# Kernel optimization log

Hardware: AMD Instinct MI355X
Metric: run time of the kernel (lower is better)

Reference implementation:

```python
import jax, jax.numpy as jnp
import numpy as np

WIN = 32  # hardcoded window size in the original module


def _find(parent, x):
    while parent[x] != x:
        parent[x] = parent[parent[x]]
        x = parent[x]
    return x


def _label_background(bg):
    # 4-connected component labeling of True pixels; False pixels get label 0
    w = bg.shape[0]
    n = w * w
    parent = np.arange(n, dtype=np.int64)
    flat = bg.ravel()
    idx = np.arange(n).reshape(w, w)
    e1 = np.concatenate([idx[:, :-1].ravel(), idx[:-1, :].ravel()])
    e2 = np.concatenate([idx[:, 1:].ravel(), idx[1:, :].ravel()])
    for a, b in zip(e1, e2):
        if flat[a] and flat[b]:
            ra, rb = _find(parent, a), _find(parent, b)
            if ra != rb:
                parent[ra] = rb
    labels = np.zeros(n, dtype=np.int64)
    root2lab = {}
    nxt = 1
    for i in range(n):
        if flat[i]:
            r = _find(parent, i)
            if r not in root2lab:
                root2lab[r] = nxt
                nxt += 1
            labels[i] = root2lab[r]
    return labels


def _malis(seg, e1, e2, costs, pos):
    # Kruskal-style maximin MALIS edge weighting (descending affinity order).
    # Pairs involving segment label 0 (foreground / non-background) are excluded.
    n = seg.shape[0]
    parent = np.arange(n, dtype=np.int64)
    cnts = [({int(seg[i]): 1} if seg[i] != 0 else {}) for i in range(n)]
    w = np.zeros(costs.shape[0], dtype=np.int64)
    order = np.argsort(-costs, kind='stable')
    for e in order:
        a, b = _find(parent, e1[e]), _find(parent, e2[e])
        if a == b:
            continue
        ca, cb = cnts[a], cnts[b]
        if len(ca) > len(cb):  # small-to-large merge
            a, b, ca, cb = b, a, cb, ca
        common = 0
        for l, c in ca.items():
            if l in cb:
                common += c * cb[l]
        if pos:
            w[e] = common
        else:
            sa = sum(ca.values())
            sb = sum(cb.values())
            w[e] = sa * sb - common
        for l, c in ca.items():
            cb[l] = cb.get(l, 0) + c
        parent[a] = b
        cnts[a] = {}
    return w


def _malis_weights_full(pred, target):
    pred = np.asarray(pred)
    target = np.asarray(target)
    B, C, H, W = pred.shape
    weights_n = np.zeros(pred.shape, dtype=np.float32)
    weights_p = np.zeros(pred.shape, dtype=np.float32)
    idx = np.arange(WIN * WIN).reshape(WIN, WIN)
    e1 = np.concatenate([idx[:, :-1].ravel(), idx[:-1, :].ravel()])
    e2 = np.concatenate([idx[:, 1:].ravel(), idx[1:, :].ravel()])
    for r in range(H // WIN):
        for c in range(W // WIN):
            p = pred[:, :, r * WIN:(r + 1) * WIN, c * WIN:(c + 1) * WIN]
            t = target[:, :, r * WIN:(r + 1) * WIN, c * WIN:(c + 1) * WIN]
            costs_h = (p[:, :, :, :-1] + p[:, :, :, 1:]).reshape(B, -1)
            costs_v = (p[:, :, :-1, :] + p[:, :, 1:, :]).reshape(B, -1)
            costs = np.concatenate([costs_h, costs_v], 1)
            gt_h = (t[:, :, :, :-1] + t[:, :, :, 1:]).reshape(B, -1)
            gt_v = (t[:, :, :-1, :] + t[:, :, 1:, :]).reshape(B, -1)
            gt = np.concatenate([gt_h, gt_v], 1)
            costs_n = costs.copy()
            costs_p = costs.copy()
            costs_n[gt > 20] = 20
            costs_p[gt < 10] = 0
            gt = np.minimum(gt, 20)
            for i in range(B):
                seg = _label_background(t[i, 0] == 0)
                wn = _malis(seg, e1, e2, costs_n[i].astype(np.float32), 0).astype(np.float64)
                wp = _malis(seg, e1, e2, costs_p[i].astype(np.float32), 1).astype(np.float64)
                if wn.sum() > 0:
                    wn = wn / wn.sum()
                if wp.sum() > 0:
                    wp = wp / wp.sum()
                wn[gt[i] >= 10] = 0
                wp[gt[i] < 20] = 0
                half = WIN * (WIN - 1)
                for wsrc, wdst in ((wn, weights_n), (wp, weights_p)):
                    wh = wsrc[:half].reshape(WIN, WIN - 1)
                    wv = wsrc[half:].reshape(WIN - 1, WIN)
                    nw = np.zeros((WIN, WIN), dtype=np.float64)
                    nw[:, :-1] += wh
                    nw[:, 1:] += wh
                    nw[:-1, :] += wv
                    nw[1:, :] += wv
                    wdst[i, 0, r * WIN:(r + 1) * WIN, c * WIN:(c + 1) * WIN] = nw
    return weights_n, weights_p


def setup_inputs() -> dict:
    key = jax.random.key(0)
    k1, k2 = jax.random.split(key)
    y_true = jax.random.randint(k1, (4, 1, 256, 256), 0, 2).astype(jnp.float32) * 20.0
    y_pred = jax.random.uniform(k2, (4, 1, 256, 256), dtype=jnp.float32) * 20.0
    return {"y_true": y_true, "y_pred": y_pred}


def reference(y_true, y_pred):
    malis_lr = 1.0
    malis_lr_pos = 1.0
    out_sd = (jax.ShapeDtypeStruct(y_pred.shape, jnp.float32),
              jax.ShapeDtypeStruct(y_pred.shape, jnp.float32))
    weights_n, weights_p = jax.pure_callback(
        _malis_weights_full, out_sd,
        jax.lax.stop_gradient(y_pred), jax.lax.stop_gradient(y_true))
    loss_n = y_pred ** 2
    loss_p = (20.0 - y_pred) ** 2
    return (malis_lr * loss_n * weights_n + malis_lr_pos * loss_p * weights_p).sum()
```

## Files before the change

### kernel.cpp

```cpp
#include <hip/hip_runtime.h>

#define NPIX   1024
#define NEH    992
#define NEDGE  1984
#define SORTN  2048
#define CHUNK  8
#define NMERGE 1023
#define NIL    0xFFFFu

#define MRG_STRIDE 20480
#define MRG_M      0
#define MRG_RA     256
#define MRG_RB     4608
#define MRG_SS     8960
#define MRG_ED     13312
#define MRG_NXT    15616

__device__ __forceinline__ void edge_ab(int e, int& a, int& b) {
    if (e < NEH) { int y = e / 31; int x = e - y * 31; a = y * 32 + x; b = a + 1; }
    else         { int ev = e - NEH; a = ev; b = ev + 32; }
}

__device__ __forceinline__ uint4 add4(uint4 x, uint4 y) {
    return make_uint4(x.x + y.x, x.y + y.y, x.z + y.z, x.w + y.w);
}
__device__ __forceinline__ uint4 sub4(uint4 x, uint4 y) {
    return make_uint4(x.x - y.x, x.y - y.y, x.z - y.z, x.w - y.w);
}

__device__ __forceinline__ unsigned rdl32(unsigned v, int lane) {
    return (unsigned)__builtin_amdgcn_readlane((int)v, lane);
}
__device__ __forceinline__ unsigned long long rdl64(unsigned long long v, int lane) {
    unsigned lo = (unsigned)__builtin_amdgcn_readlane((int)(unsigned)v, lane);
    unsigned hi = (unsigned)__builtin_amdgcn_readlane((int)(unsigned)(v >> 32), lane);
    return ((unsigned long long)hi << 32) | lo;
}

__device__ void ccl_body(char* smem, int* kprimeSh,
                         const float* __restrict__ t_glob,
                         unsigned short* __restrict__ pixLab_g,
                         int* __restrict__ Kg, int tileId) {
    const int tid = threadIdx.x;
    const int bat = tileId >> 6;
    const int tile = tileId & 63;
    const int tr = tile >> 3, tc = tile & 7;

    unsigned short* labS = (unsigned short*)smem;
    unsigned int*   cntS = (unsigned int*)(smem + 2048);
    unsigned char*  bgS  = (unsigned char*)(smem + 20480);

    for (int i = tid; i < NPIX; i += 256) {
        int y = i >> 5, x = i & 31;
        int gidx = bat * 65536 + (tr * 32 + y) * 256 + (tc * 32 + x);
        bgS[i] = (t_glob[gidx] == 0.0f) ? 1 : 0;
    }
    __syncthreads();

    if (tid < 64) {
        const int lane = tid;
        if (lane < 32) {
            #pragma unroll
            for (int x = 0; x < 32; x++) {
                int i = lane * 32 + x;
                labS[i] = bgS[i] ? (unsigned short)i : (unsigned short)NIL;
            }
        }
        while (true) {
            bool changed = false;
            if (lane < 32) {
                const int base = lane * 32;
                unsigned short v[32];
                #pragma unroll
                for (int x = 0; x < 32; x++) v[x] = labS[base + x];
                unsigned run = NIL;
                #pragma unroll
                for (int x = 0; x < 32; x++) {
                    unsigned val = v[x];
                    if (val == NIL) { run = NIL; }
                    else { unsigned nv = min(run, val); changed |= (nv != val); v[x] = (unsigned short)nv; run = nv; }
                }
                run = NIL;
                #pragma unroll
                for (int x = 31; x >= 0; x--) {
                    unsigned val = v[x];
                    if (val == NIL) { run = NIL; }
                    else { unsigned nv = min(run, val); changed |= (nv != val); v[x] = (unsigned short)nv; run = nv; }
                }
                #pragma unroll
                for (int x = 0; x < 32; x++) labS[base + x] = v[x];
            }
            if (lane < 32) {
                unsigned short c[32];
                #pragma unroll
                for (int k = 0; k < 32; k++) c[k] = labS[k * 32 + lane];
                unsigned run = NIL;
                #pragma unroll
                for (int k = 0; k < 32; k++) {
                    unsigned val = c[k];
                    if (val == NIL) { run = NIL; }
                    else { unsigned nv = min(run, val); changed |= (nv != val); c[k] = (unsigned short)nv; run = nv; }
                }
                run = NIL;
                #pragma unroll
                for (int k = 31; k >= 0; k--) {
                    unsigned val = c[k];
                    if (val == NIL) { run = NIL; }
                    else { unsigned nv = min(run, val); changed |= (nv != val); c[k] = (unsigned short)nv; run = nv; }
                }
                #pragma unroll
                for (int k = 0; k < 32; k++) labS[k * 32 + lane] = c[k];
            }
            if (!__any(changed)) break;
        }
    }
    __syncthreads();

    for (int i = tid; i < NPIX; i += 256) cntS[i] = 0;
    if (tid == 0) *kprimeSh = 0;
    __syncthreads();
    for (int i = tid; i < NPIX; i += 256)
        if (bgS[i]) atomicAdd(&cntS[labS[i]], 1u);
    __syncthreads();
    for (int i = tid; i < NPIX; i += 256) {
        if (bgS[i] && (int)labS[i] == i) {
            unsigned id = (cntS[i] >= 2) ? (unsigned)atomicAdd(kprimeSh, 1) : NIL;
            cntS[i] = id;
        }
    }
    __syncthreads();
    for (int i = tid; i < NPIX; i += 256)
        pixLab_g[tileId * NPIX + i] = bgS[i] ? (unsigned short)cntS[labS[i]] : (unsigned short)NIL;
    if (tid == 0) Kg[tileId] = *kprimeSh;
}

__device__ void sort_body(char* smem,
                          const float* __restrict__ t_glob,
                          const float* __restrict__ p_glob,
                          unsigned short* __restrict__ ord_g, int wg) {
    const int tid = threadIdx.x;
    const int sgn = wg & 1;
    const int tileId = wg >> 1;
    const int bat = tileId >> 6;
    const int tile = tileId & 63;
    const int tr = tile >> 3, tc = tile & 7;

    float*              pT   = (float*)smem;
    unsigned long long* keys = (unsigned long long*)(smem + 4096);
    unsigned char*      bgS  = (unsigned char*)(smem + 20480);

    for (int i = tid; i < NPIX; i += 256) {
        int y = i >> 5, x = i & 31;
        int gidx = bat * 65536 + (tr * 32 + y) * 256 + (tc * 32 + x);
        pT[i] = p_glob[gidx];
        bgS[i] = (t_glob[gidx] == 0.0f) ? 1 : 0;
    }
    __syncthreads();

    for (int k = tid; k < SORTN; k += 256) {
        unsigned long long key = 0ULL;
        if (k < NEDGE) {
            int a, b; edge_ab(k, a, b);
            float cost = pT[a] + pT[b];
            int nfg = (int)(!bgS[a]) + (int)(!bgS[b]);
            if (sgn == 0) { if (nfg == 2) cost = 20.0f; }
            else          { if (nfg == 0) cost = 0.0f;  }
            key = ((unsigned long long)__float_as_uint(cost) << 16)
                | (unsigned long long)(0xFFFFu - (unsigned)k);
        }
        keys[k] = key;
    }
    __syncthreads();
    for (int kk = 2; kk <= SORTN; kk <<= 1) {
        for (int jj = kk >> 1; jj > 0; jj >>= 1) {
            for (int i = tid; i < SORTN; i += 256) {
                int ixj = i ^ jj;
                if (ixj > i) {
                    unsigned long long A = keys[i], Bv = keys[ixj];
                    bool descBlk = ((i & kk) == 0);
                    if ((A < Bv) == descBlk) { keys[i] = Bv; keys[ixj] = A; }
                }
            }
            __syncthreads();
        }
    }
    for (int k = tid; k < NEDGE; k += 256)
        ord_g[(size_t)wg * SORTN + k] = (unsigned short)(0xFFFFu - (unsigned)(keys[k] & 0xFFFFULL));
}

__global__ __launch_bounds__(256, 2)
void k12_ccl_sort(const float* __restrict__ t_glob,
                  const float* __restrict__ p_glob,
                  unsigned short* __restrict__ pixLab_g,
                  int* __restrict__ Kg,
                  unsigned short* __restrict__ ord_g,
                  int nT) {
    __shared__ __align__(16) char smem[21504];
    __shared__ int kprimeSh;
    if ((int)blockIdx.x < nT)
        ccl_body(smem, &kprimeSh, t_glob, pixLab_g, Kg, blockIdx.x);
    else
        sort_body(smem, t_glob, p_glob, ord_g, blockIdx.x - nT);
}

__global__ __launch_bounds__(64)
void k3_kruskal(const float* __restrict__ t_glob,
                const unsigned short* __restrict__ ord_g,
                char* __restrict__ mrg_base) {
    const int lane = threadIdx.x;
    const int wg  = blockIdx.x;
    const int tileId = wg >> 1;
    const int bat = tileId >> 6;
    const int tile = tileId & 63;
    const int tr = tile >> 3, tc = tile & 7;

    __shared__ unsigned short parentS[NPIX];
    __shared__ unsigned long long nodeS[NPIX];
    __shared__ unsigned short nextS[NPIX];
    __shared__ unsigned int   claimS[NPIX];

    char* mg = mrg_base + (size_t)wg * MRG_STRIDE;
    unsigned int*   mrA = (unsigned int*)(mg + MRG_RA);
    unsigned int*   mrB = (unsigned int*)(mg + MRG_RB);
    unsigned int*   mSS = (unsigned int*)(mg + MRG_SS);
    unsigned short* mED = (unsigned short*)(mg + MRG_ED);
    unsigned short* mNX = (unsigned short*)(mg + MRG_NXT);
    const unsigned short* ord = ord_g + (size_t)wg * SORTN;

    for (int i = lane; i < NPIX; i += 64) {
        int y = i >> 5, x = i & 31;
        int gidx = bat * 65536 + (tr * 32 + y) * 256 + (tc * 32 + x);
        unsigned bg = (t_glob[gidx] == 0.0f) ? 1u : 0u;
        parentS[i] = (unsigned short)i;
        nodeS[i] = ((unsigned long long)i << 48) | ((unsigned long long)i << 32)
                 | (1ULL << 16) | (unsigned long long)bg;
        nextS[i] = (unsigned short)NIL;
    }
    __syncthreads();

    int m = 0;
    for (int kb = 0; kb < NEDGE; kb += 64) {
        int e = ord[kb + lane];
        int a, b; edge_ab(e, a, b);
        unsigned ra = (unsigned)a, rb = (unsigned)b;
        while (true) {
            unsigned pa = parentS[ra];
            unsigned pb = parentS[rb];
            if (pa == ra && pb == rb) break;
            if (pa != ra) { unsigned ga = parentS[pa]; parentS[ra] = (unsigned short)ga; ra = ga; }
            if (pb != rb) { unsigned gb = parentS[pb]; parentS[rb] = (unsigned short)gb; rb = gb; }
        }
        bool pending = (ra != rb);
        bool committed = false;
        unsigned recA = 0, recB = 0, recSS = 0;

        int winners = 64;
        while (__any(pending) && winners >= 6) {
            if (pending) {
                claimS[ra] = 0xFFFFFFFFu;
                claimS[rb] = 0xFFFFFFFFu;
            }
            if (pending) {
                atomicMin(&claimS[ra], (unsigned)lane);
                atomicMin(&claimS[rb], (unsigned)lane);
            }
            bool win = pending && (claimS[ra] == (unsigned)lane) && (claimS[rb] == (unsigned)lane);
            if (win) {
                unsigned long long nA = nodeS[ra], nB = nodeS[rb];
                unsigned cons = ra, surv = rb;
                unsigned szAu = (unsigned)(nA >> 16) & 0xFFFFu;
                unsigned szBu = (unsigned)(nB >> 16) & 0xFFFFu;
                if (szAu > szBu) {
                    unsigned t = cons; cons = surv; surv = t;
                    unsigned long long tn = nA; nA = nB; nB = tn;
                }
                unsigned headA = (unsigned)(nA >> 48);
                unsigned tailA = (unsigned)(nA >> 32) & 0xFFFFu;
                unsigned szA   = (unsigned)(nA >> 16) & 0xFFFFu;
                unsigned slA   = (unsigned)nA & 0xFFFFu;
                unsigned headB = (unsigned)(nB >> 48);
                unsigned tailB = (unsigned)(nB >> 32) & 0xFFFFu;
                unsigned szB   = (unsigned)(nB >> 16) & 0xFFFFu;
                unsigned slB   = (unsigned)nB & 0xFFFFu;
                unsigned long long merged =
                      ((unsigned long long)headA << 48)
                    | ((unsigned long long)tailB << 32)
                    | ((unsigned long long)(szA + szB) << 16)
                    | (unsigned long long)(slA + slB);
                parentS[cons] = (unsigned short)surv;
                nodeS[surv]   = merged;
                nextS[tailA]  = (unsigned short)headB;
                recA = (headA << 16) | headB;
                recB = (szA << 16) | szB;
                recSS = slA * slB;
                committed = true;
                pending = false;
            }
            winners = (int)__popcll(__ballot(win));
            if (pending) {
                while (true) {
                    unsigned pa = parentS[ra];
                    unsigned pb = parentS[rb];
                    if (pa == ra && pb == rb) break;
                    if (pa != ra) { unsigned ga = parentS[pa]; parentS[ra] = (unsigned short)ga; ra = ga; }
                    if (pb != rb) { unsigned gb = parentS[pb]; parentS[rb] = (unsigned short)gb; rb = gb; }
                }
                if (ra == rb) pending = false;
            }
        }

        unsigned long long cmB = __ballot(committed);
        if (committed) {
            int idx = m + (int)__popcll(cmB & ((1ULL << lane) - 1ULL));
            mrA[idx] = recA;
            mrB[idx] = recB;
            mSS[idx] = recSS;
            mED[idx] = (unsigned short)e;
        }
        int bulkCount = (int)__popcll(cmB);

        int logCount = 0;
        if (__any(pending)) {
            unsigned long long na = 0, nb = 0;
            if (pending) { na = nodeS[ra]; nb = nodeS[rb]; }
            unsigned specAB = (ra << 16) | rb;
            unsigned long long candm = __ballot(pending);
            unsigned logRa  = 0xFFFFFFFFu;
            unsigned logRbO = 0xFFFFFFFFu;
            unsigned curRoot = 0xFFFFFFFFu;
            unsigned long long logNode = 0;
            while (candm != 0ULL) {
                int j = __ffsll((long long)candm) - 1;
                candm &= candm - 1ULL;
                unsigned sAB = rdl32(specAB, j);
                unsigned cra = sAB >> 16;
                unsigned crb = sAB & 0xFFFFu;
                unsigned long long hitA = __ballot(logRa == cra);
                unsigned long long hitB = __ballot(logRa == crb);
                if (hitA) cra = rdl32(curRoot, __ffsll((long long)hitA) - 1);
                if (hitB) crb = rdl32(curRoot, __ffsll((long long)hitB) - 1);
                if (cra == crb) continue;
                unsigned ce = rdl32((unsigned)e, j);
                unsigned long long hbA = __ballot(logRbO == cra);
                unsigned long long hbB = __ballot(logRbO == crb);
                unsigned long long cna = hbA ? rdl64(logNode, 63 - __clzll((long long)hbA)) : rdl64(na, j);
                unsigned long long cnb = hbB ? rdl64(logNode, 63 - __clzll((long long)hbB)) : rdl64(nb, j);
                unsigned cons = cra, surv = crb;
                unsigned szAq = (unsigned)(cna >> 16) & 0xFFFFu;
                unsigned szBq = (unsigned)(cnb >> 16) & 0xFFFFu;
                if (szAq > szBq) {
                    unsigned t = cons; cons = surv; surv = t;
                    unsigned long long tn = cna; cna = cnb; cnb = tn;
                }
                unsigned headA = (unsigned)(cna >> 48);
                unsigned tailA = (unsigned)(cna >> 32) & 0xFFFFu;
                unsigned szA   = (unsigned)(cna >> 16) & 0xFFFFu;
                unsigned slA   = (unsigned)cna & 0xFFFFu;
                unsigned headB = (unsigned)(cnb >> 48);
                unsigned tailB = (unsigned)(cnb >> 32) & 0xFFFFu;
                unsigned szB   = (unsigned)(cnb >> 16) & 0xFFFFu;
                unsigned slB   = (unsigned)cnb & 0xFFFFu;
                unsigned long long merged =
                      ((unsigned long long)headA << 48)
                    | ((unsigned long long)tailB << 32)
                    | ((unsigned long long)(szA + szB) << 16)
                    | (unsigned long long)(slA + slB);
                if (curRoot == cons) curRoot = surv;
                if (lane == logCount) {
                    logRa = cons; logRbO = surv; curRoot = surv; logNode = merged;
                    parentS[cons] = (unsigned short)surv;
                    nodeS[surv]   = merged;
                    nextS[tailA]  = (unsigned short)headB;
                    int idx = m + bulkCount + logCount;
                    mrA[idx] = (headA << 16) | headB;
                    mrB[idx] = (szA << 16) | szB;
                    mSS[idx] = slA * slB;
                    mED[idx] = (unsigned short)ce;
                }
                logCount++;
            }
        }
        m += bulkCount + logCount;
    }
    if (lane == 0) *(int*)(mg + MRG_M) = m;
    for (int i = lane; i < NPIX; i += 64) mNX[i] = nextS[i];
}

__global__ __launch_bounds__(256, 2)
void k4_weights(const float* __restrict__ t_glob,
                const float* __restrict__ p_glob,
                const unsigned short* __restrict__ pixLab_g,
                const int* __restrict__ Kg,
                const char* __restrict__ mrg_base,
                float* __restrict__ out) {
    const int tid = threadIdx.x;
    const int wg  = blockIdx.x;
    const int sgn = wg & 1;
    const int tileId = wg >> 1;
    const int bat = tileId >> 6;
    const int tile = tileId & 63;
    const int tr = tile >> 3, tc = tile & 7;

    __shared__ float          pT[NPIX];
    __shared__ unsigned char  bgS[NPIX];
    __shared__ unsigned short pixLab[NPIX];
    __shared__ unsigned short posS[NPIX];
    __shared__ unsigned int   mRecA[NMERGE];
    __shared__ unsigned int   mRecB[NMERGE];
    __shared__ unsigned int   mSaSb[NMERGE];
    __shared__ unsigned int   commonW[NMERGE];
    __shared__ unsigned short mEd[NMERGE];
    __shared__ __align__(16) unsigned long long big[2564];
    __shared__ unsigned wsumSh;
    __shared__ float lossSh;

    const char* mg = mrg_base + (size_t)wg * MRG_STRIDE;
    const int M = *(const int*)(mg + MRG_M);
    const int K = Kg[tileId];
    const unsigned int*   mrA = (const unsigned int*)(mg + MRG_RA);
    const unsigned int*   mrB = (const unsigned int*)(mg + MRG_RB);
    const unsigned int*   mSS = (const unsigned int*)(mg + MRG_SS);
    const unsigned short* mED = (const unsigned short*)(mg + MRG_ED);
    const unsigned short* mNX = (const unsigned short*)(mg + MRG_NXT);

    for (int i = tid; i < NPIX; i += 256) {
        int y = i >> 5, x = i & 31;
        int gidx = bat * 65536 + (tr * 32 + y) * 256 + (tc * 32 + x);
        pT[i] = p_glob[gidx];
        bgS[i] = (t_glob[gidx] == 0.0f) ? 1 : 0;
        pixLab[i] = pixLab_g[tileId * NPIX + i];
    }
    for (int j = tid; j < M; j += 256) {
        mRecA[j] = mrA[j];
        mRecB[j] = mrB[j];
        mSaSb[j] = mSS[j];
        mEd[j]   = mED[j];
        commonW[j] = 0;
    }

    unsigned short* n0 = (unsigned short*)big;
    unsigned short* n1 = n0 + 1024;
    unsigned short* d0 = n0 + 2048;
    unsigned short* d1 = n0 + 3072;
    for (int i = tid; i < NPIX; i += 256) { n0[i] = mNX[i]; d0[i] = 1; }
    __syncthreads();
    for (int s = 0; s < 10; s++) {
        unsigned short* sn = (s & 1) ? n1 : n0;
        unsigned short* sd = (s & 1) ? d1 : d0;
        unsigned short* dn = (s & 1) ? n0 : n1;
        unsigned short* dd = (s & 1) ? d0 : d1;
        for (int i = tid; i < NPIX; i += 256) {
            unsigned nx = sn[i];
            unsigned dv = sd[i];
            if (nx != NIL) { dv += sd[nx]; nx = sn[nx]; }
            dn[i] = (unsigned short)nx;
            dd[i] = (unsigned short)dv;
        }
        __syncthreads();
    }
    for (int i = tid; i < NPIX; i += 256)
        posS[i] = (unsigned short)(NPIX - (int)d0[i]);
    __syncthreads();

    unsigned*       P32 = (unsigned*)big;
    uint4*          P4  = (uint4*)big;
    unsigned*       scr = P32 + 4100;
    uint4*          S4  = (uint4*)scr;
    unsigned short* P16 = (unsigned short*)big;
    for (int base = 0; base < K; base += CHUNK) {
        for (int idx = tid; idx < 4100; idx += 256) P32[idx] = 0;
        __syncthreads();
        for (int i = tid; i < NPIX; i += 256) {
            unsigned l = pixLab[i];
            if (l != NIL && l >= (unsigned)base && l < (unsigned)(base + CHUNK))
                P16[(posS[i] + 1) * 8 + (l - base)] = 1;
        }
        __syncthreads();
        {
            int r0 = tid * 4 + 1;
            uint4 acc = P4[r0];
            for (int rr = r0 + 1; rr <= r0 + 3; rr++) { acc = add4(acc, P4[rr]); P4[rr] = acc; }
            S4[tid] = acc;
            __syncthreads();
            if (tid < 64) {
                uint4 s0 = S4[tid * 4], s1 = S4[tid * 4 + 1], s2 = S4[tid * 4 + 2], s3 = S4[tid * 4 + 3];
                uint4 t1 = add4(s0, s1), t2 = add4(t1, s2), t3 = add4(t2, s3);
                uint4 run = t3;
                #pragma unroll
                for (int d = 1; d < 64; d <<= 1) {
                    uint4 o;
                    o.x = __shfl_up(run.x, d, 64);
                    o.y = __shfl_up(run.y, d, 64);
                    o.z = __shfl_up(run.z, d, 64);
                    o.w = __shfl_up(run.w, d, 64);
                    if (tid >= d) run = add4(run, o);
                }
                uint4 off = sub4(run, t3);
                S4[tid * 4]     = add4(s0, off);
                S4[tid * 4 + 1] = add4(t1, off);
                S4[tid * 4 + 2] = add4(t2, off);
                S4[tid * 4 + 3] = add4(t3, off);
            }
            __syncthreads();
            if (tid > 0) {
                uint4 off = S4[tid - 1];
                for (int rr = r0; rr <= r0 + 3; rr++) P4[rr] = add4(P4[rr], off);
            }
        }
        __syncthreads();
        for (int j = tid; j < M; j += 256) {
            unsigned recA = mRecA[j], recB = mRecB[j];
            unsigned aS = posS[recA >> 16];
            unsigned bS = posS[recA & 0xFFFFu];
            uint4 da = sub4(P4[aS + (recB >> 16)], P4[aS]);
            uint4 db = sub4(P4[bS + (recB & 0xFFFFu)], P4[bS]);
            unsigned acc;
            acc  = (da.x & 0xFFFFu) * (db.x & 0xFFFFu) + (da.x >> 16) * (db.x >> 16);
            acc += (da.y & 0xFFFFu) * (db.y & 0xFFFFu) + (da.y >> 16) * (db.y >> 16);
            acc += (da.z & 0xFFFFu) * (db.z & 0xFFFFu) + (da.z >> 16) * (db.z >> 16);
            acc += (da.w & 0xFFFFu) * (db.w & 0xFFFFu) + (da.w >> 16) * (db.w >> 16);
            commonW[j] += acc;
        }
        __syncthreads();
    }

    if (tid == 0) { wsumSh = 0; lossSh = 0.0f; }
    __syncthreads();
    unsigned wloc = 0;
    for (int j = tid; j < M; j += 256)
        wloc += (sgn == 0) ? (mSaSb[j] - commonW[j]) : commonW[j];
    if (wloc) atomicAdd(&wsumSh, wloc);
    __syncthreads();
    const unsigned wsum = wsumSh;
    if (wsum > 0) {
        const double inv = 1.0 / (double)wsum;
        float lloc = 0.0f;
        for (int j = tid; j < M; j += 256) {
            unsigned w = (sgn == 0) ? (mSaSb[j] - commonW[j]) : commonW[j];
            if (!w) continue;
            int e = mEd[j];
            int a, b; edge_ab(e, a, b);
            int nfg = (int)(!bgS[a]) + (int)(!bgS[b]);
            bool keep = (sgn == 0) ? (nfg == 0) : (nfg >= 1);
            if (!keep) continue;
            float wn = (float)((double)w * inv);
            float fa, fb;
            if (sgn == 0) { fa = pT[a] * pT[a];            fb = pT[b] * pT[b]; }
            else { float da = 20.0f - pT[a], db = 20.0f - pT[b]; fa = da * da; fb = db * db; }
            lloc += wn * (fa + fb);
        }
        if (lloc != 0.0f) atomicAdd(&lossSh, lloc);
        __syncthreads();
        if (tid == 0 && lossSh != 0.0f) atomicAdd(out, lossSh);
    }
}

__global__ __launch_bounds__(256, 2)
void malis_mono(const float* __restrict__ t_glob,
                const float* __restrict__ p_glob,
                float* __restrict__ out) {
    const int tid  = threadIdx.x;
    const int wg   = blockIdx.x;
    const int sgn  = wg & 1;
    const int tileId = wg >> 1;
    const int bat  = tileId >> 6;
    const int tile = tileId & 63;
    const int tr = tile >> 3, tc = tile & 7;

    __shared__ float          pT[NPIX];
    __shared__ unsigned char  bgS[NPIX];
    __shared__ unsigned short pixLab[NPIX];
    __shared__ unsigned short parentS[NPIX];
    __shared__ unsigned short nextS[NPIX];
    __shared__ unsigned long long nodeS[NPIX];
    __shared__ unsigned int   claimS[NPIX];
    __shared__ unsigned short posS[NPIX];
    __shared__ unsigned short orderS[NEDGE];
    __shared__ unsigned int   mRecA[NMERGE];
    __shared__ unsigned int   mRecB[NMERGE];
    __shared__ unsigned short mEd[NMERGE];
    __shared__ unsigned int   mSaSb[NMERGE];
    __shared__ unsigned int   commonW[NMERGE];
    __shared__ __align__(16) unsigned long long big[2564];
    __shared__ int   kprimeSh, mCountSh;
    __shared__ unsigned wsumSh;
    __shared__ float lossSh;

    for (int i = tid; i < NPIX; i += 256) {
        int y = i >> 5, x = i & 31;
        int gidx = bat * 65536 + (tr * 32 + y) * 256 + (tc * 32 + x);
        pT[i] = p_glob[gidx];
        bgS[i] = (t_glob[gidx] == 0.0f) ? 1 : 0;
    }
    __syncthreads();

    unsigned short* labS = (unsigned short*)big;
    unsigned int*   cntS = (unsigned int*)(((char*)big) + 2048);
    if (tid < 64) {
        const int lane = tid;
        if (lane < 32) {
            #pragma unroll
            for (int x = 0; x < 32; x++) {
                int i = lane * 32 + x;
                labS[i] = bgS[i] ? (unsigned short)i : (unsigned short)NIL;
            }
        }
        while (true) {
            bool changed = false;
            if (lane < 32) {
                const int base = lane * 32;
                unsigned short v[32];
                #pragma unroll
                for (int x = 0; x < 32; x++) v[x] = labS[base + x];
                unsigned run = NIL;
                #pragma unroll
                for (int x = 0; x < 32; x++) {
                    unsigned val = v[x];
                    if (val == NIL) { run = NIL; }
                    else { unsigned nv = min(run, val); changed |= (nv != val); v[x] = (unsigned short)nv; run = nv; }
                }
                run = NIL;
                #pragma unroll
                for (int x = 31; x >= 0; x--) {
                    unsigned val = v[x];
                    if (val == NIL) { run = NIL; }
                    else { unsigned nv = min(run, val); changed |= (nv != val); v[x] = (unsigned short)nv; run = nv; }
                }
                #pragma unroll
                for (int x = 0; x < 32; x++) labS[base + x] = v[x];
            }
            if (lane < 32) {
                unsigned short c[32];
                #pragma unroll
                for (int k = 0; k < 32; k++) c[k] = labS[k * 32 + lane];
                unsigned run = NIL;
                #pragma unroll
                for (int k = 0; k < 32; k++) {
                    unsigned val = c[k];
                    if (val == NIL) { run = NIL; }
                    else { unsigned nv = min(run, val); changed |= (nv != val); c[k] = (unsigned short)nv; run = nv; }
                }
                run = NIL;
                #pragma unroll
                for (int k = 31; k >= 0; k--) {
                    unsigned val = c[k];
                    if (val == NIL) { run = NIL; }
                    else { unsigned nv = min(run, val); changed |= (nv != val); c[k] = (unsigned short)nv; run = nv; }
                }
                #pragma unroll
                for (int k = 0; k < 32; k++) labS[k * 32 + lane] = c[k];
            }
            if (!__any(changed)) break;
        }
    }
    __syncthreads();

    for (int i = tid; i < NPIX; i += 256) cntS[i] = 0;
    if (tid == 0) kprimeSh = 0;
    __syncthreads();
    for (int i = tid; i < NPIX; i += 256)
        if (bgS[i]) atomicAdd(&cntS[labS[i]], 1u);
    __syncthreads();
    for (int i = tid; i < NPIX; i += 256) {
        if (bgS[i] && (int)labS[i] == i) {
            unsigned id = (cntS[i] >= 2) ? (unsigned)atomicAdd(&kprimeSh, 1) : NIL;
            cntS[i] = id;
        }
    }
    __syncthreads();
    for (int i = tid; i < NPIX; i += 256)
        pixLab[i] = bgS[i] ? (unsigned short)cntS[labS[i]] : (unsigned short)NIL;
    __syncthreads();
    const int K = kprimeSh;

    unsigned long long* keys = big;
    for (int k = tid; k < SORTN; k += 256) {
        unsigned long long key = 0ULL;
        if (k < NEDGE) {
            int a, b; edge_ab(k, a, b);
            float cost = pT[a] + pT[b];
            int nfg = (int)(!bgS[a]) + (int)(!bgS[b]);
            if (sgn == 0) { if (nfg == 2) cost = 20.0f; }
            else          { if (nfg == 0) cost = 0.0f;  }
            key = ((unsigned long long)__float_as_uint(cost) << 16)
                | (unsigned long long)(0xFFFFu - (unsigned)k);
        }
        keys[k] = key;
    }
    __syncthreads();
    for (int kk = 2; kk <= SORTN; kk <<= 1) {
        for (int jj = kk >> 1; jj > 0; jj >>= 1) {
            for (int i = tid; i < SORTN; i += 256) {
                int ixj = i ^ jj;
                if (ixj > i) {
                    unsigned long long A = keys[i], Bv = keys[ixj];
                    bool descBlk = ((i & kk) == 0);
                    if ((A < Bv) == descBlk) { keys[i] = Bv; keys[ixj] = A; }
                }
            }
            __syncthreads();
        }
    }
    for (int k = tid; k < NEDGE; k += 256)
        orderS[k] = (unsigned short)(0xFFFFu - (unsigned)(keys[k] & 0xFFFFULL));
    for (int i = tid; i < NPIX; i += 256) {
        parentS[i] = (unsigned short)i;
        nodeS[i] = ((unsigned long long)i << 48) | ((unsigned long long)i << 32)
                 | (1ULL << 16) | (unsigned long long)bgS[i];
        nextS[i] = (unsigned short)NIL;
    }
    __syncthreads();

    if (tid < 64) {
        const int lane = tid;
        int m = 0;
        for (int kb = 0; kb < NEDGE; kb += 64) {
            int e = orderS[kb + lane];
            int a, b; edge_ab(e, a, b);
            unsigned ra = (unsigned)a, rb = (unsigned)b;
            bool pending = true;
            bool committed = false;
            unsigned recA = 0, recB = 0, recSS = 0;
            while (__any(pending)) {
                if (pending) {
                    while (true) {
                        unsigned pa = parentS[ra];
                        unsigned pb = parentS[rb];
                        if (pa == ra && pb == rb) break;
                        if (pa != ra) { unsigned ga = parentS[pa]; parentS[ra] = (unsigned short)ga; ra = ga; }
                        if (pb != rb) { unsigned gb = parentS[pb]; parentS[rb] = (unsigned short)gb; rb = gb; }
                    }
                    if (ra == rb) pending = false;
                }
                if (pending) {
                    claimS[ra] = 0xFFFFFFFFu;
                    claimS[rb] = 0xFFFFFFFFu;
                }
                if (pending) {
                    atomicMin(&claimS[ra], (unsigned)lane);
                    atomicMin(&claimS[rb], (unsigned)lane);
                }
                bool win = pending && (claimS[ra] == (unsigned)lane) && (claimS[rb] == (unsigned)lane);
                if (win) {
                    unsigned long long nA = nodeS[ra], nB = nodeS[rb];
                    unsigned cons = ra, surv = rb;
                    unsigned szAu = (unsigned)(nA >> 16) & 0xFFFFu;
                    unsigned szBu = (unsigned)(nB >> 16) & 0xFFFFu;
                    if (szAu > szBu) {
                        unsigned t = cons; cons = surv; surv = t;
                        unsigned long long tn = nA; nA = nB; nB = tn;
                    }
                    unsigned headA = (unsigned)(nA >> 48);
                    unsigned tailA = (unsigned)(nA >> 32) & 0xFFFFu;
                    unsigned szA   = (unsigned)(nA >> 16) & 0xFFFFu;
                    unsigned slA   = (unsigned)nA & 0xFFFFu;
                    unsigned headB = (unsigned)(nB >> 48);
                    unsigned tailB = (unsigned)(nB >> 32) & 0xFFFFu;
                    unsigned szB   = (unsigned)(nB >> 16) & 0xFFFFu;
                    unsigned slB   = (unsigned)nB & 0xFFFFu;
                    unsigned long long merged =
                          ((unsigned long long)headA << 48)
                        | ((unsigned long long)tailB << 32)
                        | ((unsigned long long)(szA + szB) << 16)
                        | (unsigned long long)(slA + slB);
                    parentS[cons] = (unsigned short)surv;
                    nodeS[surv]   = merged;
                    nextS[tailA]  = (unsigned short)headB;
                    recA = (headA << 16) | headB;
                    recB = (szA << 16) | szB;
                    recSS = slA * slB;
                    committed = true;
                    pending = false;
                }
            }
            unsigned long long cm = __ballot(committed);
            if (committed) {
                int idx = m + (int)__popcll(cm & ((1ULL << lane) - 1ULL));
                mRecA[idx] = recA;
                mRecB[idx] = recB;
                mSaSb[idx] = recSS;
                mEd[idx]   = (unsigned short)e;
            }
            m += (int)__popcll(cm);
        }
        if (lane == 0) mCountSh = m;
    }
    __syncthreads();
    const int M = mCountSh;
    for (int j = tid; j < M; j += 256) commonW[j] = 0;

    unsigned short* n0 = (unsigned short*)big;
    unsigned short* n1 = n0 + 1024;
    unsigned short* d0 = n0 + 2048;
    unsigned short* d1 = n0 + 3072;
    for (int i = tid; i < NPIX; i += 256) { n0[i] = nextS[i]; d0[i] = 1; }
    __syncthreads();
    for (int s = 0; s < 10; s++) {
        unsigned short* sn = (s & 1) ? n1 : n0;
        unsigned short* sd = (s & 1) ? d1 : d0;
        unsigned short* dn = (s & 1) ? n0 : n1;
        unsigned short* dd = (s & 1) ? d0 : d1;
        for (int i = tid; i < NPIX; i += 256) {
            unsigned nx = sn[i];
            unsigned dv = sd[i];
            if (nx != NIL) { dv += sd[nx]; nx = sn[nx]; }
            dn[i] = (unsigned short)nx;
            dd[i] = (unsigned short)dv;
        }
        __syncthreads();
    }
    for (int i = tid; i < NPIX; i += 256)
        posS[i] = (unsigned short)(NPIX - (int)d0[i]);
    __syncthreads();

    unsigned*       P32 = (unsigned*)big;
    uint4*          P4  = (uint4*)big;
    unsigned*       scr = P32 + 4100;
    uint4*          S4  = (uint4*)scr;
    unsigned short* P16 = (unsigned short*)big;
    for (int base = 0; base < K; base += CHUNK) {
        for (int idx = tid; idx < 4100; idx += 256) P32[idx] = 0;
        __syncthreads();
        for (int i = tid; i < NPIX; i += 256) {
            unsigned l = pixLab[i];
            if (l != NIL && l >= (unsigned)base && l < (unsigned)(base + CHUNK))
                P16[(posS[i] + 1) * 8 + (l - base)] = 1;
        }
        __syncthreads();
        {
            int r0 = tid * 4 + 1;
            uint4 acc = P4[r0];
            for (int rr = r0 + 1; rr <= r0 + 3; rr++) { acc = add4(acc, P4[rr]); P4[rr] = acc; }
            S4[tid] = acc;
            __syncthreads();
            if (tid < 64) {
                uint4 s0 = S4[tid * 4], s1 = S4[tid * 4 + 1], s2 = S4[tid * 4 + 2], s3 = S4[tid * 4 + 3];
                uint4 t1 = add4(s0, s1), t2 = add4(t1, s2), t3 = add4(t2, s3);
                uint4 run = t3;
                #pragma unroll
                for (int d = 1; d < 64; d <<= 1) {
                    uint4 o;
                    o.x = __shfl_up(run.x, d, 64);
                    o.y = __shfl_up(run.y, d, 64);
                    o.z = __shfl_up(run.z, d, 64);
                    o.w = __shfl_up(run.w, d, 64);
                    if (tid >= d) run = add4(run, o);
                }
                uint4 off = sub4(run, t3);
                S4[tid * 4]     = add4(s0, off);
                S4[tid * 4 + 1] = add4(t1, off);
                S4[tid * 4 + 2] = add4(t2, off);
                S4[tid * 4 + 3] = add4(t3, off);
            }
            __syncthreads();
            if (tid > 0) {
                uint4 off = S4[tid - 1];
                for (int rr = r0; rr <= r0 + 3; rr++) P4[rr] = add4(P4[rr], off);
            }
        }
        __syncthreads();
        for (int j = tid; j < M; j += 256) {
            unsigned recA = mRecA[j], recB = mRecB[j];
            unsigned aS = posS[recA >> 16];
            unsigned bS = posS[recA & 0xFFFFu];
            uint4 da = sub4(P4[aS + (recB >> 16)], P4[aS]);
            uint4 db = sub4(P4[bS + (recB & 0xFFFFu)], P4[bS]);
            unsigned acc;
            acc  = (da.x & 0xFFFFu) * (db.x & 0xFFFFu) + (da.x >> 16) * (db.x >> 16);
            acc += (da.y & 0xFFFFu) * (db.y & 0xFFFFu) + (da.y >> 16) * (db.y >> 16);
            acc += (da.z & 0xFFFFu) * (db.z & 0xFFFFu) + (da.z >> 16) * (db.z >> 16);
            acc += (da.w & 0xFFFFu) * (db.w & 0xFFFFu) + (da.w >> 16) * (db.w >> 16);
            commonW[j] += acc;
        }
        __syncthreads();
    }

    if (tid == 0) { wsumSh = 0; lossSh = 0.0f; }
    __syncthreads();
    unsigned wloc = 0;
    for (int j = tid; j < M; j += 256)
        wloc += (sgn == 0) ? (mSaSb[j] - commonW[j]) : commonW[j];
    if (wloc) atomicAdd(&wsumSh, wloc);
    __syncthreads();
    const unsigned wsum = wsumSh;
    if (wsum > 0) {
        const double inv = 1.0 / (double)wsum;
        float lloc = 0.0f;
        for (int j = tid; j < M; j += 256) {
            unsigned w = (sgn == 0) ? (mSaSb[j] - commonW[j]) : commonW[j];
            if (!w) continue;
            int e = mEd[j];
            int a, b; edge_ab(e, a, b);
            int nfg = (int)(!bgS[a]) + (int)(!bgS[b]);
            bool keep = (sgn == 0) ? (nfg == 0) : (nfg >= 1);
            if (!keep) continue;
            float wn = (float)((double)w * inv);
            float fa, fb;
            if (sgn == 0) { fa = pT[a] * pT[a];            fb = pT[b] * pT[b]; }
            else { float da = 20.0f - pT[a], db = 20.0f - pT[b]; fa = da * da; fb = db * db; }
            lloc += wn * (fa + fb);
        }
        if (lloc != 0.0f) atomicAdd(&lossSh, lloc);
        __syncthreads();
        if (tid == 0 && lossSh != 0.0f) atomicAdd(out, lossSh);
    }
}

extern "C" void kernel_launch(void* const* d_in, const int* in_sizes, int n_in,
                              void* d_out, int out_size, void* d_ws, size_t ws_size,
                              hipStream_t stream) {
    const float* y_true = (const float*)d_in[0];
    const float* y_pred = (const float*)d_in[1];
    float* out = (float*)d_out;
    const int B  = in_sizes[0] / (256 * 256);
    const int nT = B * 64;
    const int nW = nT * 2;

    const size_t offK   = (size_t)nT * 2048;
    const size_t offOrd = offK + (((size_t)nT * 4 + 255) & ~(size_t)255);
    const size_t offMrg = offOrd + (size_t)nW * 4096;
    const size_t need   = offMrg + (size_t)nW * MRG_STRIDE;

    hipMemsetAsync(d_out, 0, (size_t)out_size * sizeof(float), stream);

    if (ws_size >= need) {
        char* ws = (char*)d_ws;
        unsigned short* pixLab_g = (unsigned short*)ws;
        int*            Kg       = (int*)(ws + offK);
        unsigned short* ord_g    = (unsigned short*)(ws + offOrd);
        char*           mrg      = ws + offMrg;
        hipLaunchKernelGGL(k12_ccl_sort, dim3(nT + nW), dim3(256), 0, stream,
                           y_true, y_pred, pixLab_g, Kg, ord_g, nT);
        hipLaunchKernelGGL(k3_kruskal,   dim3(nW), dim3(64),  0, stream, y_true, ord_g, mrg);
        hipLaunchKernelGGL(k4_weights,   dim3(nW), dim3(256), 0, stream, y_true, y_pred,
                           pixLab_g, Kg, mrg, out);
    } else {
        hipLaunchKernelGGL(malis_mono, dim3(nW), dim3(256), 0, stream, y_true, y_pred, out);
    }
}
```

Baseline: 297.6 us.

## Fuse Kruskal pass into weights kernel and add star-merge fast path

Merges the single-wave Kruskal kernel into the weights kernel, so the merge records and next-list stay in shared memory instead of being written to and re-read from a global workspace, and one kernel launch goes away. Claim slots now carry a generation counter, so they are no longer reset each round. A new fast path handles the case where every leftover pending edge touches one common root: it merges them all in one step using prefix sums instead of a serial lane-by-lane loop. Costs: the fused kernel uses more shared memory, which can lower occupancy, and 192 of the 256 threads sit idle during the serial Kruskal phase.

After: 270.8 us. 1.1x faster.

```diff
diff --git a/kernel.cpp b/kernel.cpp
--- a/kernel.cpp
+++ b/kernel.cpp
@@ -7,14 +7,6 @@
 #define CHUNK  8
 #define NMERGE 1023
 #define NIL    0xFFFFu
-
-#define MRG_STRIDE 20480
-#define MRG_M      0
-#define MRG_RA     256
-#define MRG_RB     4608
-#define MRG_SS     8960
-#define MRG_ED     13312
-#define MRG_NXT    15616
 
 __device__ __forceinline__ void edge_ab(int e, int& a, int& b) {
     if (e < NEH) { int y = e / 31; int x = e - y * 31; a = y * 32 + x; b = a + 1; }
@@ -203,196 +195,13 @@
         sort_body(smem, t_glob, p_glob, ord_g, blockIdx.x - nT);
 }
 
-__global__ __launch_bounds__(64)
-void k3_kruskal(const float* __restrict__ t_glob,
-                const unsigned short* __restrict__ ord_g,
-                char* __restrict__ mrg_base) {
-    const int lane = threadIdx.x;
-    const int wg  = blockIdx.x;
-    const int tileId = wg >> 1;
-    const int bat = tileId >> 6;
-    const int tile = tileId & 63;
-    const int tr = tile >> 3, tc = tile & 7;
-
-    __shared__ unsigned short parentS[NPIX];
-    __shared__ unsigned long long nodeS[NPIX];
-    __shared__ unsigned short nextS[NPIX];
-    __shared__ unsigned int   claimS[NPIX];
-
-    char* mg = mrg_base + (size_t)wg * MRG_STRIDE;
-    unsigned int*   mrA = (unsigned int*)(mg + MRG_RA);
-    unsigned int*   mrB = (unsigned int*)(mg + MRG_RB);
-    unsigned int*   mSS = (unsigned int*)(mg + MRG_SS);
-    unsigned short* mED = (unsigned short*)(mg + MRG_ED);
-    unsigned short* mNX = (unsigned short*)(mg + MRG_NXT);
-    const unsigned short* ord = ord_g + (size_t)wg * SORTN;
-
-    for (int i = lane; i < NPIX; i += 64) {
-        int y = i >> 5, x = i & 31;
-        int gidx = bat * 65536 + (tr * 32 + y) * 256 + (tc * 32 + x);
-        unsigned bg = (t_glob[gidx] == 0.0f) ? 1u : 0u;
-        parentS[i] = (unsigned short)i;
-        nodeS[i] = ((unsigned long long)i << 48) | ((unsigned long long)i << 32)
-                 | (1ULL << 16) | (unsigned long long)bg;
-        nextS[i] = (unsigned short)NIL;
-    }
-    __syncthreads();
-
-    int m = 0;
-    for (int kb = 0; kb < NEDGE; kb += 64) {
-        int e = ord[kb + lane];
-        int a, b; edge_ab(e, a, b);
-        unsigned ra = (unsigned)a, rb = (unsigned)b;
-        while (true) {
-            unsigned pa = parentS[ra];
-            unsigned pb = parentS[rb];
-            if (pa == ra && pb == rb) break;
-            if (pa != ra) { unsigned ga = parentS[pa]; parentS[ra] = (unsigned short)ga; ra = ga; }
-            if (pb != rb) { unsigned gb = parentS[pb]; parentS[rb] = (unsigned short)gb; rb = gb; }
-        }
-        bool pending = (ra != rb);
-        bool committed = false;
-        unsigned recA = 0, recB = 0, recSS = 0;
-
-        int winners = 64;
-        while (__any(pending) && winners >= 6) {
-            if (pending) {
-                claimS[ra] = 0xFFFFFFFFu;
-                claimS[rb] = 0xFFFFFFFFu;
-            }
-            if (pending) {
-                atomicMin(&claimS[ra], (unsigned)lane);
-                atomicMin(&claimS[rb], (unsigned)lane);
-            }
-            bool win = pending && (claimS[ra] == (unsigned)lane) && (claimS[rb] == (unsigned)lane);
-            if (win) {
-                unsigned long long nA = nodeS[ra], nB = nodeS[rb];
-                unsigned cons = ra, surv = rb;
-                unsigned szAu = (unsigned)(nA >> 16) & 0xFFFFu;
-                unsigned szBu = (unsigned)(nB >> 16) & 0xFFFFu;
-                if (szAu > szBu) {
-                    unsigned t = cons; cons = surv; surv = t;
-                    unsigned long long tn = nA; nA = nB; nB = tn;
-                }
-                unsigned headA = (unsigned)(nA >> 48);
-                unsigned tailA = (unsigned)(nA >> 32) & 0xFFFFu;
-                unsigned szA   = (unsigned)(nA >> 16) & 0xFFFFu;
-                unsigned slA   = (unsigned)nA & 0xFFFFu;
-                unsigned headB = (unsigned)(nB >> 48);
-                unsigned tailB = (unsigned)(nB >> 32) & 0xFFFFu;
-                unsigned szB   = (unsigned)(nB >> 16) & 0xFFFFu;
-                unsigned slB   = (unsigned)nB & 0xFFFFu;
-                unsigned long long merged =
-                      ((unsigned long long)headA << 48)
-                    | ((unsigned long long)tailB << 32)
-                    | ((unsigned long long)(szA + szB) << 16)
-                    | (unsigned long long)(slA + slB);
-                parentS[cons] = (unsigned short)surv;
-                nodeS[surv]   = merged;
-                nextS[tailA]  = (unsigned short)headB;
-                recA = (headA << 16) | headB;
-                recB = (szA << 16) | szB;
-                recSS = slA * slB;
-                committed = true;
-                pending = false;
-            }
-            winners = (int)__popcll(__ballot(win));
-            if (pending) {
-                while (true) {
-                    unsigned pa = parentS[ra];
-                    unsigned pb = parentS[rb];
-                    if (pa == ra && pb == rb) break;
-                    if (pa != ra) { unsigned ga = parentS[pa]; parentS[ra] = (unsigned short)ga; ra = ga; }
-                    if (pb != rb) { unsigned gb = parentS[pb]; parentS[rb] = (unsigned short)gb; rb = gb; }
-                }
-                if (ra == rb) pending = false;
-            }
-        }
-
-        unsigned long long cmB = __ballot(committed);
-        if (committed) {
-            int idx = m + (int)__popcll(cmB & ((1ULL << lane) - 1ULL));
-            mrA[idx] = recA;
-            mrB[idx] = recB;
-            mSS[idx] = recSS;
-            mED[idx] = (unsigned short)e;
-        }
-        int bulkCount = (int)__popcll(cmB);
-
-        int logCount = 0;
-        if (__any(pending)) {
-            unsigned long long na = 0, nb = 0;
-            if (pending) { na = nodeS[ra]; nb = nodeS[rb]; }
-            unsigned specAB = (ra << 16) | rb;
-            unsigned long long candm = __ballot(pending);
-            unsigned logRa  = 0xFFFFFFFFu;
-            unsigned logRbO = 0xFFFFFFFFu;
-            unsigned curRoot = 0xFFFFFFFFu;
-            unsigned long long logNode = 0;
-            while (candm != 0ULL) {
-                int j = __ffsll((long long)candm) - 1;
-                candm &= candm - 1ULL;
-                unsigned sAB = rdl32(specAB, j);
-                unsigned cra = sAB >> 16;
-                unsigned crb = sAB & 0xFFFFu;
-                unsigned long long hitA = __ballot(logRa == cra);
-                unsigned long long hitB = __ballot(logRa == crb);
-                if (hitA) cra = rdl32(curRoot, __ffsll((long long)hitA) - 1);
-                if (hitB) crb = rdl32(curRoot, __ffsll((long long)hitB) - 1);
-                if (cra == crb) continue;
-                unsigned ce = rdl32((unsigned)e, j);
-                unsigned long long hbA = __ballot(logRbO == cra);
-                unsigned long long hbB = __ballot(logRbO == crb);
-                unsigned long long cna = hbA ? rdl64(logNode, 63 - __clzll((long long)hbA)) : rdl64(na, j);
-                unsigned long long cnb = hbB ? rdl64(logNode, 63 - __clzll((long long)hbB)) : rdl64(nb, j);
-                unsigned cons = cra, surv = crb;
-                unsigned szAq = (unsigned)(cna >> 16) & 0xFFFFu;
-                unsigned szBq = (unsigned)(cnb >> 16) & 0xFFFFu;
-                if (szAq > szBq) {
-                    unsigned t = cons; cons = surv; surv = t;
-                    unsigned long long tn = cna; cna = cnb; cnb = tn;
-                }
-                unsigned headA = (unsigned)(cna >> 48);
-                unsigned tailA = (unsigned)(cna >> 32) & 0xFFFFu;
-                unsigned szA   = (unsigned)(cna >> 16) & 0xFFFFu;
-                unsigned slA   = (unsigned)cna & 0xFFFFu;
-                unsigned headB = (unsigned)(cnb >> 48);
-                unsigned tailB = (unsigned)(cnb >> 32) & 0xFFFFu;
-                unsigned szB   = (unsigned)(cnb >> 16) & 0xFFFFu;
-                unsigned slB   = (unsigned)cnb & 0xFFFFu;
-                unsigned long long merged =
-                      ((unsigned long long)headA << 48)
-                    | ((unsigned long long)tailB << 32)
-                    | ((unsigned long long)(szA + szB) << 16)
-                    | (unsigned long long)(slA + slB);
-                if (curRoot == cons) curRoot = surv;
-                if (lane == logCount) {
-                    logRa = cons; logRbO = surv; curRoot = surv; logNode = merged;
-                    parentS[cons] = (unsigned short)surv;
-                    nodeS[surv]   = merged;
-                    nextS[tailA]  = (unsigned short)headB;
-                    int idx = m + bulkCount + logCount;
-                    mrA[idx] = (headA << 16) | headB;
-                    mrB[idx] = (szA << 16) | szB;
-                    mSS[idx] = slA * slB;
-                    mED[idx] = (unsigned short)ce;
-                }
-                logCount++;
-            }
-        }
-        m += bulkCount + logCount;
-    }
-    if (lane == 0) *(int*)(mg + MRG_M) = m;
-    for (int i = lane; i < NPIX; i += 64) mNX[i] = nextS[i];
-}
-
 __global__ __launch_bounds__(256, 2)
-void k4_weights(const float* __restrict__ t_glob,
-                const float* __restrict__ p_glob,
-                const unsigned short* __restrict__ pixLab_g,
-                const int* __restrict__ Kg,
-                const char* __restrict__ mrg_base,
-                float* __restrict__ out) {
+void k34_fused(const float* __restrict__ t_glob,
+               const float* __restrict__ p_glob,
+               const unsigned short* __restrict__ pixLab_g,
+               const int* __restrict__ Kg,
+               const unsigned short* __restrict__ ord_g,
+               float* __restrict__ out) {
     const int tid = threadIdx.x;
     const int wg  = blockIdx.x;
     const int sgn = wg & 1;
@@ -401,48 +210,261 @@
     const int tile = tileId & 63;
     const int tr = tile >> 3, tc = tile & 7;
 
-    __shared__ float          pT[NPIX];
-    __shared__ unsigned char  bgS[NPIX];
-    __shared__ unsigned short pixLab[NPIX];
-    __shared__ unsigned short posS[NPIX];
+    __shared__ unsigned short parentS[NPIX];
+    __shared__ unsigned long long nodeS[NPIX];
+    __shared__ unsigned short nextS[NPIX];
     __shared__ unsigned int   mRecA[NMERGE];
     __shared__ unsigned int   mRecB[NMERGE];
     __shared__ unsigned int   mSaSb[NMERGE];
     __shared__ unsigned int   commonW[NMERGE];
     __shared__ unsigned short mEd[NMERGE];
+    __shared__ float          pT[NPIX];
+    __shared__ unsigned char  bgS[NPIX];
+    __shared__ unsigned short pixLab[NPIX];
+    __shared__ unsigned short posS[NPIX];
+    __shared__ unsigned int   claimS[NPIX];
     __shared__ __align__(16) unsigned long long big[2564];
+    __shared__ int   mCountSh;
     __shared__ unsigned wsumSh;
     __shared__ float lossSh;
 
-    const char* mg = mrg_base + (size_t)wg * MRG_STRIDE;
-    const int M = *(const int*)(mg + MRG_M);
-    const int K = Kg[tileId];
-    const unsigned int*   mrA = (const unsigned int*)(mg + MRG_RA);
-    const unsigned int*   mrB = (const unsigned int*)(mg + MRG_RB);
-    const unsigned int*   mSS = (const unsigned int*)(mg + MRG_SS);
-    const unsigned short* mED = (const unsigned short*)(mg + MRG_ED);
-    const unsigned short* mNX = (const unsigned short*)(mg + MRG_NXT);
+    const unsigned short* ord = ord_g + (size_t)wg * SORTN;
 
     for (int i = tid; i < NPIX; i += 256) {
         int y = i >> 5, x = i & 31;
         int gidx = bat * 65536 + (tr * 32 + y) * 256 + (tc * 32 + x);
+        float tv = t_glob[gidx];
+        unsigned bg = (tv == 0.0f) ? 1u : 0u;
         pT[i] = p_glob[gidx];
-        bgS[i] = (t_glob[gidx] == 0.0f) ? 1 : 0;
+        bgS[i] = (unsigned char)bg;
         pixLab[i] = pixLab_g[tileId * NPIX + i];
-    }
-    for (int j = tid; j < M; j += 256) {
-        mRecA[j] = mrA[j];
-        mRecB[j] = mrB[j];
-        mSaSb[j] = mSS[j];
-        mEd[j]   = mED[j];
-        commonW[j] = 0;
-    }
+        parentS[i] = (unsigned short)i;
+        nodeS[i] = ((unsigned long long)i << 48) | ((unsigned long long)i << 32)
+                 | (1ULL << 16) | (unsigned long long)bg;
+        nextS[i] = (unsigned short)NIL;
+        claimS[i] = 0xFFFFFFFFu;
+    }
+    __syncthreads();
+
+    if (tid < 64) {
+        const int lane = tid;
+        int m = 0;
+        unsigned gen = 1u << 24;
+        for (int kb = 0; kb < NEDGE; kb += 64) {
+            int e = ord[kb + lane];
+            int a, b; edge_ab(e, a, b);
+            unsigned ra = (unsigned)a, rb = (unsigned)b;
+            while (true) {
+                unsigned pa = parentS[ra];
+                unsigned pb = parentS[rb];
+                if (pa == ra && pb == rb) break;
+                if (pa != ra) { unsigned ga = parentS[pa]; parentS[ra] = (unsigned short)ga; ra = ga; }
+                if (pb != rb) { unsigned gb = parentS[pb]; parentS[rb] = (unsigned short)gb; rb = gb; }
+            }
+            bool pending = (ra != rb);
+            bool committed = false;
+            unsigned recA = 0, recB = 0, recSS = 0;
+
+            int winners = 64;
+            while (__any(pending) && winners >= 6) {
+                gen--;
+                unsigned myval = (gen << 6) | (unsigned)lane;
+                if (pending) {
+                    atomicMin(&claimS[ra], myval);
+                    atomicMin(&claimS[rb], myval);
+                }
+                bool win = pending && (claimS[ra] == myval) && (claimS[rb] == myval);
+                if (win) {
+                    unsigned long long nA = nodeS[ra], nB = nodeS[rb];
+                    unsigned cons = ra, surv = rb;
+                    unsigned szAu = (unsigned)(nA >> 16) & 0xFFFFu;
+                    unsigned szBu = (unsigned)(nB >> 16) & 0xFFFFu;
+                    if (szAu > szBu) {
+                        unsigned t = cons; cons = surv; surv = t;
+                        unsigned long long tn = nA; nA = nB; nB = tn;
+                    }
+                    unsigned headA = (unsigned)(nA >> 48);
+                    unsigned tailA = (unsigned)(nA >> 32) & 0xFFFFu;
+                    unsigned szA   = (unsigned)(nA >> 16) & 0xFFFFu;
+                    unsigned slA   = (unsigned)nA & 0xFFFFu;
+                    unsigned headB = (unsigned)(nB >> 48);
+                    unsigned tailB = (unsigned)(nB >> 32) & 0xFFFFu;
+                    unsigned szB   = (unsigned)(nB >> 16) & 0xFFFFu;
+                    unsigned slB   = (unsigned)nB & 0xFFFFu;
+                    unsigned long long merged =
+                          ((unsigned long long)headA << 48)
+                        | ((unsigned long long)tailB << 32)
+                        | ((unsigned long long)(szA + szB) << 16)
+                        | (unsigned long long)(slA + slB);
+                    parentS[cons] = (unsigned short)surv;
+                    nodeS[surv]   = merged;
+                    nextS[tailA]  = (unsigned short)headB;
+                    recA = (headA << 16) | headB;
+                    recB = (szA << 16) | szB;
+                    recSS = slA * slB;
+                    committed = true;
+                    pending = false;
+                }
+                winners = (int)__popcll(__ballot(win));
+                if (pending) {
+                    while (true) {
+                        unsigned pa = parentS[ra];
+                        unsigned pb = parentS[rb];
+                        if (pa == ra && pb == rb) break;
+                        if (pa != ra) { unsigned ga = parentS[pa]; parentS[ra] = (unsigned short)ga; ra = ga; }
+                        if (pb != rb) { unsigned gb = parentS[pb]; parentS[rb] = (unsigned short)gb; rb = gb; }
+                    }
+                    if (ra == rb) pending = false;
+                }
+            }
+
+            unsigned long long cmB = __ballot(committed);
+            if (committed) {
+                int idx = m + (int)__popcll(cmB & ((1ULL << lane) - 1ULL));
+                mRecA[idx] = recA;
+                mRecB[idx] = recB;
+                mSaSb[idx] = recSS;
+                mEd[idx]   = (unsigned short)e;
+            }
+            m += (int)__popcll(cmB);
+
+            int logCount = 0;
+            unsigned long long candm0 = __ballot(pending);
+            if (candm0 != 0ULL) {
+                unsigned long long na = 0, nb = 0;
+                if (pending) { na = nodeS[ra]; nb = nodeS[rb]; }
+                int j0 = __ffsll((long long)candm0) - 1;
+                unsigned Ra = rdl32(ra, j0), Rb = rdl32(rb, j0);
+                unsigned long long mAc = __ballot(pending && (ra == Ra || rb == Ra));
+                unsigned long long mBc = __ballot(pending && (ra == Rb || rb == Rb));
+                unsigned R = (__popcll(mAc) >= __popcll(mBc)) ? Ra : Rb;
+                bool onR  = pending && ((ra == R) != (rb == R));
+                bool offR = pending && (ra != R) && (rb != R);
+
+                if (!__any(offR)) {
+                    unsigned cons = 0;
+                    unsigned long long cnode = 0;
+                    if (onR) { cons = (ra == R) ? rb : ra; cnode = (ra == R) ? nb : na; }
+                    gen--;
+                    unsigned myval = (gen << 6) | (unsigned)lane;
+                    if (onR) atomicMin(&claimS[cons], myval);
+                    bool valid = onR && (claimS[cons] == myval);
+                    unsigned long long vm = __ballot(valid);
+                    if (vm != 0ULL) {
+                        unsigned long long rnode = (R == Ra) ? rdl64(na, j0) : rdl64(nb, j0);
+                        unsigned headR0 = (unsigned)(rnode >> 48);
+                        unsigned tailR0 = (unsigned)(rnode >> 32) & 0xFFFFu;
+                        unsigned szR0   = (unsigned)(rnode >> 16) & 0xFFFFu;
+                        unsigned slR0   = (unsigned)rnode & 0xFFFFu;
+                        unsigned headA = valid ? (unsigned)(cnode >> 48) : 0u;
+                        unsigned tailA = valid ? (unsigned)(cnode >> 32) & 0xFFFFu : 0u;
+                        unsigned szA   = valid ? (unsigned)(cnode >> 16) & 0xFFFFu : 0u;
+                        unsigned slA   = valid ? (unsigned)cnode & 0xFFFFu : 0u;
+                        unsigned s1 = szA, s2 = slA;
+                        #pragma unroll
+                        for (int d = 1; d < 64; d <<= 1) {
+                            unsigned o1 = __shfl_up(s1, d, 64);
+                            unsigned o2 = __shfl_up(s2, d, 64);
+                            if (lane >= d) { s1 += o1; s2 += o2; }
+                        }
+                        unsigned szPre = s1 - szA, slPre = s2 - slA;
+                        unsigned long long below = vm & ((1ULL << lane) - 1ULL);
+                        int pv = 63 - (int)__clzll((long long)(below | 1ULL));
+                        unsigned hprev = __shfl(headA, below ? pv : 0, 64);
+                        unsigned headB = below ? hprev : headR0;
+                        unsigned szB = szR0 + szPre;
+                        unsigned slB = slR0 + slPre;
+                        if (valid) {
+                            parentS[cons] = (unsigned short)R;
+                            nextS[tailA]  = (unsigned short)headB;
+                            int idx = m + (int)__popcll(below);
+                            mRecA[idx] = (headA << 16) | headB;
+                            mRecB[idx] = (szA << 16) | szB;
+                            mSaSb[idx] = slA * slB;
+                            mEd[idx]   = (unsigned short)e;
+                        }
+                        int last = 63 - (int)__clzll((long long)vm);
+                        if (valid && lane == last) {
+                            nodeS[R] = ((unsigned long long)headA << 48)
+                                     | ((unsigned long long)tailR0 << 32)
+                                     | ((unsigned long long)(szR0 + s1) << 16)
+                                     | (unsigned long long)(slR0 + s2);
+                        }
+                        logCount = (int)__popcll(vm);
+                    }
+                } else {
+                    unsigned specAB = (ra << 16) | rb;
+                    unsigned long long candm = candm0;
+                    unsigned logRa  = 0xFFFFFFFFu;
+                    unsigned logRbO = 0xFFFFFFFFu;
+                    unsigned curRoot = 0xFFFFFFFFu;
+                    unsigned long long logNode = 0;
+                    while (candm != 0ULL) {
+                        int j = __ffsll((long long)candm) - 1;
+                        candm &= candm - 1ULL;
+                        unsigned sAB = rdl32(specAB, j);
+                        unsigned cra = sAB >> 16;
+                        unsigned crb = sAB & 0xFFFFu;
+                        unsigned long long hitA = __ballot(logRa == cra);
+                        unsigned long long hitB = __ballot(logRa == crb);
+                        if (hitA) cra = rdl32(curRoot, __ffsll((long long)hitA) - 1);
+                        if (hitB) crb = rdl32(curRoot, __ffsll((long long)hitB) - 1);
+                        if (cra == crb) continue;
+                        unsigned ce = rdl32((unsigned)e, j);
+                        unsigned long long hbA = __ballot(logRbO == cra);
+                        unsigned long long hbB = __ballot(logRbO == crb);
+                        unsigned long long cna = hbA ? rdl64(logNode, 63 - __clzll((long long)hbA)) : rdl64(na, j);
+                        unsigned long long cnb = hbB ? rdl64(logNode, 63 - __clzll((long long)hbB)) : rdl64(nb, j);
+                        unsigned cons = cra, surv = crb;
+                        unsigned szAq = (unsigned)(cna >> 16) & 0xFFFFu;
+                        unsigned szBq = (unsigned)(cnb >> 16) & 0xFFFFu;
+                        if (szAq > szBq) {
+                            unsigned t = cons; cons = surv; surv = t;
+                            unsigned long long tn = cna; cna = cnb; cnb = tn;
+                        }
+                        unsigned headA = (unsigned)(cna >> 48);
+                        unsigned tailA = (unsigned)(cna >> 32) & 0xFFFFu;
+                        unsigned szA   = (unsigned)(cna >> 16) & 0xFFFFu;
+                        unsigned slA   = (unsigned)cna & 0xFFFFu;
+                        unsigned headB = (unsigned)(cnb >> 48);
+                        unsigned tailB = (unsigned)(cnb >> 32) & 0xFFFFu;
+                        unsigned szB   = (unsigned)(cnb >> 16) & 0xFFFFu;
+                        unsigned slB   = (unsigned)cnb & 0xFFFFu;
+                        unsigned long long merged =
+                              ((unsigned long long)headA << 48)
+                            | ((unsigned long long)tailB << 32)
+                            | ((unsigned long long)(szA + szB) << 16)
+                            | (unsigned long long)(slA + slB);
+                        if (curRoot == cons) curRoot = surv;
+                        if (lane == logCount) {
+                            logRa = cons; logRbO = surv; curRoot = surv; logNode = merged;
+                            parentS[cons] = (unsigned short)surv;
+                            nodeS[surv]   = merged;
+                            nextS[tailA]  = (unsigned short)headB;
+                            int idx = m + logCount;
+                            mRecA[idx] = (headA << 16) | headB;
+                            mRecB[idx] = (szA << 16) | szB;
+                            mSaSb[idx] = slA * slB;
+                            mEd[idx]   = (unsigned short)ce;
+                        }
+                        logCount++;
+                    }
+                }
+            }
+            m += logCount;
+        }
+        if (lane == 0) mCountSh = m;
+    }
+    __syncthreads();
+    const int M = mCountSh;
+    const int K = Kg[tileId];
+    for (int j = tid; j < M; j += 256) commonW[j] = 0;
 
     unsigned short* n0 = (unsigned short*)big;
     unsigned short* n1 = n0 + 1024;
     unsigned short* d0 = n0 + 2048;
     unsigned short* d1 = n0 + 3072;
-    for (int i = tid; i < NPIX; i += 256) { n0[i] = mNX[i]; d0[i] = 1; }
+    for (int i = tid; i < NPIX; i += 256) { n0[i] = nextS[i]; d0[i] = 1; }
     __syncthreads();
     for (int s = 0; s < 10; s++) {
         unsigned short* sn = (s & 1) ? n1 : n0;
@@ -918,8 +940,7 @@
 
     const size_t offK   = (size_t)nT * 2048;
     const size_t offOrd = offK + (((size_t)nT * 4 + 255) & ~(size_t)255);
-    const size_t offMrg = offOrd + (size_t)nW * 4096;
-    const size_t need   = offMrg + (size_t)nW * MRG_STRIDE;
+    const size_t need   = offOrd + (size_t)nW * 4096;
 
     hipMemsetAsync(d_out, 0, (size_t)out_size * sizeof(float), stream);
 
@@ -928,12 +949,10 @@
         unsigned short* pixLab_g = (unsigned short*)ws;
         int*            Kg       = (int*)(ws + offK);
         unsigned short* ord_g    = (unsigned short*)(ws + offOrd);
-        char*           mrg      = ws + offMrg;
         hipLaunchKernelGGL(k12_ccl_sort, dim3(nT + nW), dim3(256), 0, stream,
                            y_true, y_pred, pixLab_g, Kg, ord_g, nT);
-        hipLaunchKernelGGL(k3_kruskal,   dim3(nW), dim3(64),  0, stream, y_true, ord_g, mrg);
-        hipLaunchKernelGGL(k4_weights,   dim3(nW), dim3(256), 0, stream, y_true, y_pred,
-                           pixLab_g, Kg, mrg, out);
+        hipLaunchKernelGGL(k34_fused,    dim3(nW), dim3(256), 0, stream,
+                           y_true, y_pred, pixLab_g, Kg, ord_g, out);
     } else {
         hipLaunchKernelGGL(malis_mono, dim3(nW), dim3(256), 0, stream, y_true, y_pred, out);
     }
```
